# Kernel tuning notes

Hardware: AMD Instinct MI355X
Metric: run time of the kernel (lower is better)

## Reference

```python
import jax, jax.numpy as jnp
import numpy as np

C = 768
H = 12
HD = C // H  # 64


def setup_inputs() -> dict:
    key = jax.random.key(0)
    k1, k2, k3, k4, k5, k6 = jax.random.split(key, 6)
    B, T = 8, 1024
    x = jax.random.normal(k1, (B, T, C), dtype=jnp.float32)
    mask = jax.random.randint(k2, (B, T), 0, 2, dtype=jnp.int32)
    # Linear params stored so that y = x @ W + b (W is [in, out])
    W_attn = jax.random.normal(k3, (C, 3 * C), dtype=jnp.float32) * 0.02
    b_attn = jax.random.normal(k4, (3 * C,), dtype=jnp.float32) * 0.02
    W_proj = jax.random.normal(k5, (C, C), dtype=jnp.float32) * 0.02
    b_proj = jax.random.normal(k6, (C,), dtype=jnp.float32) * 0.02
    return {"x": x, "mask": mask, "W_attn": W_attn, "b_attn": b_attn,
            "W_proj": W_proj, "b_proj": b_proj}


def reference(x, mask, W_attn, b_attn, W_proj, b_proj):
    B, T, _ = x.shape
    qkv = x @ W_attn + b_attn                      # [B, T, 3C]
    q, k, v = jnp.split(qkv, 3, axis=2)            # each [B, T, C]
    # [B, T, C] -> [B, H, T, HD]
    q = q.reshape(B, T, H, HD).transpose(0, 2, 1, 3)
    k = k.reshape(B, T, H, HD).transpose(0, 2, 1, 3)
    v = v.reshape(B, T, H, HD).transpose(0, 2, 1, 3)

    scale = 1.0 / np.sqrt(HD).astype(np.float32)
    att = jnp.einsum('bhqd,bhkd->bhqk', q, k) * scale  # [B, H, T, T]

    causal = jnp.tril(jnp.ones((T, T), dtype=bool))    # [T, T]
    att = jnp.where(causal[None, None], att, -jnp.inf)

    # custom mask: per-(batch, query-row) flag; where mask==0 the whole row
    # of scores is overwritten with 0.0001 (AFTER causal fill, as in torch)
    row_masked = (mask == 0)[:, None, :, None]         # [B, 1, T, 1]
    att = jnp.where(row_masked, jnp.float32(1e-4), att)

    att = jax.nn.softmax(att, axis=-1)
    # dropout layers are identity in eval mode
    y = jnp.einsum('bhqk,bhkd->bhqd', att, v)          # [B, H, T, HD]
    y = y.transpose(0, 2, 1, 3).reshape(B, T, C)
    y = y @ W_proj + b_proj
    return y
```

## Files before the change

kernel.cpp:

```cpp
#include <hip/hip_runtime.h>

#define BQ 8
#define TT 1024
#define CC 768
#define NH 12
#define HD 64
#define BH (BQ*NH)
#define MROWS (BQ*TT)
#define NQKV (3*CC)
#define KD CC

typedef unsigned short u16;
typedef __attribute__((ext_vector_type(4))) short short4v;
typedef __attribute__((ext_vector_type(8))) short short8v;
typedef __attribute__((ext_vector_type(4))) float floatx4;
typedef __attribute__((address_space(1))) const unsigned int gu32;
typedef __attribute__((address_space(3))) unsigned int lu32;

__device__ __forceinline__ float bf2f(u16 u) {
  union { unsigned int i; float f; } c; c.i = ((unsigned int)u) << 16; return c.f;
}
__device__ __forceinline__ u16 f2bf(float f) {
  union { float f; unsigned int i; } c; c.f = f;
  unsigned int i = c.i;
  return (u16)((i + 0x7FFFu + ((i >> 16) & 1u)) >> 16);
}
__device__ __forceinline__ float fast_exp2(float x) {
  return __builtin_amdgcn_exp2f(x);
}
__device__ __forceinline__ void async_ld16(const u16* g, u16* l) {
  __builtin_amdgcn_global_load_lds((gu32*)g, (lu32*)l, 16, 0, 0);
}

#define PREP_CONV 6144
#define PREP_WA   1728

__global__ __launch_bounds__(256) void prep_kernel(
    const float* __restrict__ x, u16* __restrict__ xb,
    const float* __restrict__ Wattn, u16* __restrict__ WtA,
    const float* __restrict__ Wproj, u16* __restrict__ WtP)
{
  __shared__ float tile[32][33];
  int bid = blockIdx.x;
  int tid = threadIdx.x;
  if (bid < PREP_CONV) {
    int i = (bid * 256 + tid) * 4;
    floatx4 v = *(const floatx4*)(x + i);
    short4v o;
    o[0] = (short)f2bf(v[0]); o[1] = (short)f2bf(v[1]);
    o[2] = (short)f2bf(v[2]); o[3] = (short)f2bf(v[3]);
    *(short4v*)(xb + i) = o;
    return;
  }
  const float* in; u16* out; int R, Cc, b2;
  if (bid < PREP_CONV + PREP_WA) { in = Wattn; out = WtA; R = KD; Cc = NQKV; b2 = bid - PREP_CONV; }
  else                           { in = Wproj; out = WtP; R = CC; Cc = CC;   b2 = bid - PREP_CONV - PREP_WA; }
  int ct = Cc >> 5;
  int bx = b2 % ct;
  int by = b2 / ct;
  int tx = tid & 31;
  int ty = tid >> 5;
  int c0 = bx << 5, r0 = by << 5;
#pragma unroll
  for (int s = 0; s < 4; ++s)
    tile[ty + s*8][tx] = in[(size_t)(r0 + ty + s*8) * Cc + c0 + tx];
  __syncthreads();
#pragma unroll
  for (int s = 0; s < 4; ++s)
    out[(size_t)(c0 + ty + s*8) * R + r0 + tx] = f2bf(tile[tx][ty + s*8]);
}

__global__ __launch_bounds__(256) void gemm_bt(
    const u16* __restrict__ A, const u16* __restrict__ Bt,
    const float* __restrict__ bias,
    float* __restrict__ out,
    u16* __restrict__ qo, u16* __restrict__ ko, u16* __restrict__ vo,
    int M, int N, int mode)
{
  __shared__ u16 As[64 * 64];
  __shared__ u16 Bs[128 * 64];

  int tid = threadIdx.x;
  int lane = tid & 63;
  int w = tid >> 6;
  int c = lane & 15;
  int q4 = lane >> 4;

  int mtiles = M >> 6;
  int mt = blockIdx.x % mtiles;
  int nt = blockIdx.x / mtiles;
  int m0 = mt << 6, n0 = nt << 7;

  int wr = (w >> 1) << 5;
  int wc = (w & 1) << 6;

  int srow8 = lane >> 3;
  int ug = ((lane & 7) ^ srow8) << 3;
  const u16* ag = A  + (size_t)(m0 + w * 16 + srow8) * KD + ug;
  const u16* bg = Bt + (size_t)(n0 + w * 32 + srow8) * KD + ug;
  u16* asl = &As[(w * 16) * 64];
  u16* bsl = &Bs[(w * 32) * 64];

  floatx4 acc[2][4];
#pragma unroll
  for (int mi = 0; mi < 2; ++mi)
#pragma unroll
    for (int ni = 0; ni < 4; ++ni) acc[mi][ni] = (floatx4){0.f, 0.f, 0.f, 0.f};

  int c7 = c & 7;

#pragma unroll 1
  for (int kt = 0; kt < KD; kt += 64) {
    async_ld16(ag + kt,              asl);
    async_ld16(ag + kt + 8 * KD,     asl + 8 * 64);
    async_ld16(bg + kt,              bsl);
    async_ld16(bg + kt + 8 * KD,     bsl + 8 * 64);
    async_ld16(bg + kt + 16 * KD,    bsl + 16 * 64);
    async_ld16(bg + kt + 24 * KD,    bsl + 24 * 64);
    __syncthreads();

    short8v af[2][2], bf[4][2];
#pragma unroll
    for (int kc = 0; kc < 2; ++kc) {
      int uoff = ((kc * 4 + q4) ^ c7) << 3;
#pragma unroll
      for (int mi = 0; mi < 2; ++mi)
        af[mi][kc] = *(const short8v*)&As[(wr + mi * 16 + c) * 64 + uoff];
#pragma unroll
      for (int ni = 0; ni < 4; ++ni)
        bf[ni][kc] = *(const short8v*)&Bs[(wc + ni * 16 + c) * 64 + uoff];
    }
#pragma unroll
    for (int kc = 0; kc < 2; ++kc)
#pragma unroll
      for (int mi = 0; mi < 2; ++mi)
#pragma unroll
        for (int ni = 0; ni < 4; ++ni)
          acc[mi][ni] = __builtin_amdgcn_mfma_f32_16x16x32_bf16(af[mi][kc], bf[ni][kc], acc[mi][ni], 0, 0, 0);
    __syncthreads();
  }

  if (mode == 0) {
    int which = (n0 + wc) / CC;
    int nbase = (n0 + wc) - which * CC;
    u16* dst0 = (which == 0) ? qo : ((which == 1) ? ko : vo);
#pragma unroll
    for (int ni = 0; ni < 4; ++ni) {
      int nn = nbase + ni * 16 + c;
      int hh = nn >> 6, dd = nn & 63;
      float bv = bias[which * CC + nn];
#pragma unroll
      for (int mi = 0; mi < 2; ++mi) {
#pragma unroll
        for (int r = 0; r < 4; ++r) {
          int mm = m0 + wr + mi * 16 + q4 * 4 + r;
          int bb = mm >> 10, tt = mm & 1023;
          size_t idx = (((size_t)(bb * NH + hh)) * TT + tt) * HD + dd;
          dst0[idx] = f2bf(acc[mi][ni][r] + bv);
        }
      }
    }
  } else {
#pragma unroll
    for (int ni = 0; ni < 4; ++ni) {
      int nn = n0 + wc + ni * 16 + c;
      float bv = bias[nn];
#pragma unroll
      for (int mi = 0; mi < 2; ++mi) {
#pragma unroll
        for (int r = 0; r < 4; ++r) {
          int mm = m0 + wr + mi * 16 + q4 * 4 + r;
          out[(size_t)mm * N + nn] = acc[mi][ni][r] + bv;
        }
      }
    }
  }
}

__global__ __launch_bounds__(256) void transpose_v(
    const u16* __restrict__ vb, u16* __restrict__ vt)
{
  __shared__ u16 tile[64][72];
  int tid = threadIdx.x;
  int tt0 = (blockIdx.x & 15) << 6;
  int bh = blockIdx.x >> 4;
  {
    int trow = tid >> 2;
    int dchunk = (tid & 3) << 4;
    const u16* src = vb + (((size_t)bh * TT + tt0 + trow) * HD) + dchunk;
    *(short8v*)&tile[trow][dchunk]     = *(const short8v*)src;
    *(short8v*)&tile[trow][dchunk + 8] = *(const short8v*)(src + 8);
  }
  __syncthreads();
  {
    int drow = tid >> 2;
    int tchunk = (tid & 3) << 4;
    short8v a, bv;
#pragma unroll
    for (int j = 0; j < 8; ++j) {
      a[j]  = (short)tile[tchunk + j][drow];
      bv[j] = (short)tile[tchunk + 8 + j][drow];
    }
    u16* dst = vt + ((size_t)bh * HD + drow) * TT + tt0 + tchunk;
    *(short8v*)dst       = a;
    *(short8v*)(dst + 8) = bv;
  }
}

__global__ __launch_bounds__(256) void vk_stats(
    const u16* __restrict__ vtb, const u16* __restrict__ kb,
    float* __restrict__ mv, float* __restrict__ kmaxn)
{
  __shared__ float red[256];
  int bh = blockIdx.x;
  int tid = threadIdx.x;
  int d = tid & 63;
  int g4 = tid >> 6;

  {
    const u16* vp = vtb + ((size_t)bh * HD + d) * TT + g4 * 256;
    float s = 0.f;
#pragma unroll 4
    for (int j = 0; j < 256; j += 8) {
      short8v v = *(const short8v*)(vp + j);
#pragma unroll
      for (int i = 0; i < 8; ++i) s += bf2f((u16)v[i]);
    }
    red[tid] = s;
  }
  __syncthreads();
  if (g4 == 0) mv[bh * HD + d] = (red[d] + red[d + 64] + red[d + 128] + red[d + 192]) * (1.0f / 1024.0f);
  __syncthreads();

  float mx = 0.f;
#pragma unroll 1
  for (int t = tid; t < TT; t += 256) {
    const u16* p = kb + ((size_t)bh * TT + t) * HD;
    float ss = 0.f;
#pragma unroll
    for (int j = 0; j < 64; j += 8) {
      short8v v = *(const short8v*)(p + j);
#pragma unroll
      for (int i = 0; i < 8; ++i) {
        float f = bf2f((u16)v[i]);
        ss = fmaf(f, f, ss);
      }
    }
    mx = fmaxf(mx, ss);
  }
  red[tid] = mx;
  __syncthreads();
  for (int s2 = 128; s2 > 0; s2 >>= 1) {
    if (tid < s2) red[tid] = fmaxf(red[tid], red[tid + s2]);
    __syncthreads();
  }
  if (tid == 0) kmaxn[bh] = sqrtf(red[0]);
}

#define LDW 72
#define SCL 0.18033688f

__global__ __launch_bounds__(256) void attn_kernel(
    const u16* __restrict__ qb, const u16* __restrict__ kb,
    const u16* __restrict__ vtb, const int* __restrict__ mask,
    const float* __restrict__ meanv, const float* __restrict__ kmaxn,
    u16* __restrict__ outb)
{
  __shared__ u16 Ks[64 * LDW];
  __shared__ u16 Vs[64 * LDW];
  __shared__ u16 Ps[4][16 * LDW];

  int tid = threadIdx.x;
  int lane = tid & 63;
  int w = tid >> 6;
  int c = lane & 15;
  int q4 = lane >> 4;

  int pair = blockIdx.x & 7;
  int bh = blockIdx.x >> 3;
  int b = bh / NH;
  int h = bh - b * NH;
  float kmax = kmaxn[bh];

  int srow = tid >> 2;
  int schunk = (tid & 3) << 4;
  const u16* kgp = kb + ((size_t)bh * TT + srow) * HD + schunk;
  const u16* vgp = vtb + ((size_t)bh * HD + srow) * TT + schunk;
  u16* ksw = &Ks[srow * LDW + schunk];
  u16* vsw = &Vs[srow * LDW + schunk];
  u16* pw = &Ps[w][0];

  short8v onesv;
#pragma unroll
  for (int j = 0; j < 8; ++j) onesv[j] = (short)0x3F80;

#pragma unroll 1
  for (int phase = 0; phase < 2; ++phase) {
    int qt = phase ? (15 - pair) : pair;
    int rowbase = (qt << 6) + (w << 4);

    short8v qfrag[2];
    {
      const u16* qp = qb + ((size_t)bh * TT + rowbase + c) * HD + q4 * 8;
      qfrag[0] = *(const short8v*)qp;
      qfrag[1] = *(const short8v*)(qp + 32);
    }

    float q2 = 0.f;
#pragma unroll
    for (int kc = 0; kc < 2; ++kc)
#pragma unroll
      for (int j = 0; j < 8; ++j) {
        float qv = bf2f((u16)qfrag[kc][j]);
        q2 = fmaf(qv, qv, q2);
      }
    q2 += __shfl_xor(q2, 16);
    q2 += __shfl_xor(q2, 32);
    float Mc = sqrtf(q2) * kmax * SCL;

    floatx4 o[4];
#pragma unroll
    for (int i = 0; i < 4; ++i) o[i] = (floatx4){0.f, 0.f, 0.f, 0.f};
    floatx4 o5 = (floatx4){0.f, 0.f, 0.f, 0.f};

    short8v kr0, kr1, vr0, vr1;
    kr0 = *(const short8v*)kgp;
    kr1 = *(const short8v*)(kgp + 8);
    vr0 = *(const short8v*)vgp;
    vr1 = *(const short8v*)(vgp + 8);

#pragma unroll 1
    for (int kt = 0; kt <= qt; ++kt) {
      __syncthreads();
      *(short8v*)ksw = kr0; *(short8v*)(ksw + 8) = kr1;
      *(short8v*)vsw = vr0; *(short8v*)(vsw + 8) = vr1;
      __syncthreads();

      if (kt < qt) {
        const u16* kp = kgp + ((size_t)(kt + 1) << 6) * HD;
        const u16* vp = vgp + ((kt + 1) << 6);
        kr0 = *(const short8v*)kp;
        kr1 = *(const short8v*)(kp + 8);
        vr0 = *(const short8v*)vp;
        vr1 = *(const short8v*)(vp + 8);
      }

      floatx4 s[4];
#pragma unroll
      for (int nt = 0; nt < 4; ++nt) s[nt] = (floatx4){0.f, 0.f, 0.f, 0.f};
#pragma unroll
      for (int kc = 0; kc < 2; ++kc) {
#pragma unroll
        for (int nt = 0; nt < 4; ++nt) {
          short8v kf = *(const short8v*)&Ks[(nt * 16 + c) * LDW + kc * 32 + q4 * 8];
          s[nt] = __builtin_amdgcn_mfma_f32_16x16x32_bf16(kf, qfrag[kc], s[nt], 0, 0, 0);
        }
      }

      int qrl = (w << 4) + c;
#pragma unroll
      for (int nt = 0; nt < 4; ++nt) {
        short4v pk;
#pragma unroll
        for (int r = 0; r < 4; ++r) {
          float sv = s[nt][r];
          if (kt == qt && (nt * 16 + (q4 << 2) + r > qrl)) sv = -INFINITY;
          pk[r] = (short)f2bf(fast_exp2(fmaf(sv, SCL, -Mc)));
        }
        *(short4v*)&pw[c * LDW + nt * 16 + (q4 << 2)] = pk;
      }

#pragma unroll
      for (int kc = 0; kc < 2; ++kc) {
        short8v pf = *(const short8v*)&pw[c * LDW + kc * 32 + q4 * 8];
#pragma unroll
        for (int nt = 0; nt < 4; ++nt) {
          short8v vf = *(const short8v*)&Vs[(nt * 16 + c) * LDW + kc * 32 + q4 * 8];
          o[nt] = __builtin_amdgcn_mfma_f32_16x16x32_bf16(pf, vf, o[nt], 0, 0, 0);
        }
        o5 = __builtin_amdgcn_mfma_f32_16x16x32_bf16(pf, onesv, o5, 0, 0, 0);
      }
    }

    int qrow[4]; bool msk[4]; float inv[4];
#pragma unroll
    for (int r = 0; r < 4; ++r) {
      qrow[r] = rowbase + q4 * 4 + r;
      msk[r] = (mask[b * TT + qrow[r]] == 0);
      inv[r] = 1.f / o5[r];
    }
#pragma unroll
    for (int nt = 0; nt < 4; ++nt) {
      int d = nt * 16 + c;
      float mv = meanv[bh * HD + d];
#pragma unroll
      for (int r = 0; r < 4; ++r) {
        float val = msk[r] ? mv : o[nt][r] * inv[r];
        outb[((size_t)(b * TT + qrow[r])) * CC + h * HD + d] = f2bf(val);
      }
    }
  }
}

extern "C" void kernel_launch(void* const* d_in, const int* in_sizes, int n_in,
                              void* d_out, int out_size, void* d_ws, size_t ws_size,
                              hipStream_t stream)
{
  (void)in_sizes; (void)n_in; (void)out_size; (void)ws_size;
  const float* x     = (const float*)d_in[0];
  const int*   mask  = (const int*)d_in[1];
  const float* Wattn = (const float*)d_in[2];
  const float* battn = (const float*)d_in[3];
  const float* Wproj = (const float*)d_in[4];
  const float* bproj = (const float*)d_in[5];
  float* out = (float*)d_out;

  char* ws = (char*)d_ws;
  size_t off = 0;
  auto alloc = [&](size_t bytes) -> void* {
    void* p = ws + off;
    off += (bytes + 255) & ~(size_t)255;
    return p;
  };
  u16* WtA  = (u16*)alloc((size_t)NQKV * KD * 2);
  u16* WtP  = (u16*)alloc((size_t)CC * CC * 2);
  u16* xb   = (u16*)alloc((size_t)MROWS * CC * 2);
  u16* qbuf = (u16*)alloc((size_t)MROWS * CC * 2);
  u16* kbuf = (u16*)alloc((size_t)MROWS * CC * 2);
  u16* vbuf = (u16*)alloc((size_t)MROWS * CC * 2);
  u16* vtb  = (u16*)alloc((size_t)MROWS * CC * 2);
  u16* abuf = (u16*)alloc((size_t)MROWS * CC * 2);
  float* mv = (float*)alloc((size_t)BH * HD * 4);
  float* kmx = (float*)alloc((size_t)BH * 4);

  prep_kernel<<<8448, 256, 0, stream>>>(x, xb, Wattn, WtA, Wproj, WtP);

  gemm_bt<<<(MROWS/64)*(NQKV/128), 256, 0, stream>>>(
      xb, WtA, battn, nullptr, qbuf, kbuf, vbuf, MROWS, NQKV, 0);

  transpose_v<<<BH * (TT/64), 256, 0, stream>>>(vbuf, vtb);
  vk_stats<<<BH, 256, 0, stream>>>(vtb, kbuf, mv, kmx);

  attn_kernel<<<BH * 8, 256, 0, stream>>>(qbuf, kbuf, vtb, mask, mv, kmx, abuf);

  gemm_bt<<<(MROWS/64)*(CC/128), 256, 0, stream>>>(
      abuf, WtP, bproj, out, nullptr, nullptr, nullptr, MROWS, CC, 1);
}
```

Measured before the change: 200.9 us.

## Fuse V transpose with stats, double-buffer attention K/V, add specialized proj GEMM

```diff
diff --git a/kernel.cpp b/kernel.cpp
--- a/kernel.cpp
+++ b/kernel.cpp
@@ -34,15 +34,23 @@
 
 #define PREP_CONV 6144
 #define PREP_WA   1728
+#define PREP_WP   576
+#define PREP_TOTAL (PREP_CONV + PREP_WA + PREP_WP)
 
 __global__ __launch_bounds__(256) void prep_kernel(
     const float* __restrict__ x, u16* __restrict__ xb,
     const float* __restrict__ Wattn, u16* __restrict__ WtA,
-    const float* __restrict__ Wproj, u16* __restrict__ WtP)
+    const float* __restrict__ Wproj, u16* __restrict__ WtP,
+    float* __restrict__ mvz, unsigned int* __restrict__ kmxz)
 {
   __shared__ float tile[32][33];
   int bid = blockIdx.x;
   int tid = threadIdx.x;
+  if (bid == PREP_TOTAL) {
+    for (int i = tid; i < BH * HD; i += 256) mvz[i] = 0.f;
+    if (tid < BH) kmxz[tid] = 0u;
+    return;
+  }
   if (bid < PREP_CONV) {
     int i = (bid * 256 + tid) * 4;
     floatx4 v = *(const floatx4*)(x + i);
@@ -177,13 +185,101 @@
   }
 }
 
-__global__ __launch_bounds__(256) void transpose_v(
-    const u16* __restrict__ vb, u16* __restrict__ vt)
+__global__ __launch_bounds__(256) void gemm_proj(
+    const u16* __restrict__ A, const u16* __restrict__ Bt,
+    const float* __restrict__ bias, float* __restrict__ out)
+{
+  __shared__ u16 As[64 * 128];
+  __shared__ u16 Bs[128 * 128];
+
+  int tid = threadIdx.x;
+  int lane = tid & 63;
+  int w = tid >> 6;
+  int c = lane & 15;
+  int q4 = lane >> 4;
+
+  int mt = blockIdx.x & 127;
+  int nt = blockIdx.x >> 7;
+  int m0 = mt << 6, n0 = nt << 7;
+
+  int wr = (w >> 1) << 5;
+  int wc = (w & 1) << 6;
+
+  int srow4 = lane >> 4;
+  int u16i = lane & 15;
+
+  floatx4 acc[2][4];
+#pragma unroll
+  for (int mi = 0; mi < 2; ++mi)
+#pragma unroll
+    for (int ni = 0; ni < 4; ++ni) acc[mi][ni] = (floatx4){0.f, 0.f, 0.f, 0.f};
+
+#pragma unroll 1
+  for (int kt = 0; kt < KD; kt += 128) {
+#pragma unroll
+    for (int i = 0; i < 4; ++i) {
+      int row = w * 16 + i * 4 + srow4;
+      async_ld16(A + (size_t)(m0 + row) * KD + kt + ((u16i ^ (row & 15)) << 3),
+                 &As[(w * 16 + i * 4) * 128]);
+    }
+#pragma unroll
+    for (int i = 0; i < 8; ++i) {
+      int row = w * 32 + i * 4 + srow4;
+      async_ld16(Bt + (size_t)(n0 + row) * KD + kt + ((u16i ^ (row & 15)) << 3),
+                 &Bs[(w * 32 + i * 4) * 128]);
+    }
+    __syncthreads();
+
+#pragma unroll
+    for (int kc = 0; kc < 4; ++kc) {
+      int uoff = (((kc << 2) + q4) ^ c) << 3;
+      short8v af0 = *(const short8v*)&As[(wr + c) * 128 + uoff];
+      short8v af1 = *(const short8v*)&As[(wr + 16 + c) * 128 + uoff];
+      short8v bf0 = *(const short8v*)&Bs[(wc + c) * 128 + uoff];
+      short8v bf1 = *(const short8v*)&Bs[(wc + 16 + c) * 128 + uoff];
+      short8v bf2 = *(const short8v*)&Bs[(wc + 32 + c) * 128 + uoff];
+      short8v bf3 = *(const short8v*)&Bs[(wc + 48 + c) * 128 + uoff];
+      acc[0][0] = __builtin_amdgcn_mfma_f32_16x16x32_bf16(af0, bf0, acc[0][0], 0, 0, 0);
+      acc[0][1] = __builtin_amdgcn_mfma_f32_16x16x32_bf16(af0, bf1, acc[0][1], 0, 0, 0);
+      acc[0][2] = __builtin_amdgcn_mfma_f32_16x16x32_bf16(af0, bf2, acc[0][2], 0, 0, 0);
+      acc[0][3] = __builtin_amdgcn_mfma_f32_16x16x32_bf16(af0, bf3, acc[0][3], 0, 0, 0);
+      acc[1][0] = __builtin_amdgcn_mfma_f32_16x16x32_bf16(af1, bf0, acc[1][0], 0, 0, 0);
+      acc[1][1] = __builtin_amdgcn_mfma_f32_16x16x32_bf16(af1, bf1, acc[1][1], 0, 0, 0);
+      acc[1][2] = __builtin_amdgcn_mfma_f32_16x16x32_bf16(af1, bf2, acc[1][2], 0, 0, 0);
+      acc[1][3] = __builtin_amdgcn_mfma_f32_16x16x32_bf16(af1, bf3, acc[1][3], 0, 0, 0);
+    }
+    __syncthreads();
+  }
+
+#pragma unroll
+  for (int ni = 0; ni < 4; ++ni) {
+    int nn = n0 + wc + ni * 16 + c;
+    float bv = bias[nn];
+#pragma unroll
+    for (int mi = 0; mi < 2; ++mi) {
+#pragma unroll
+      for (int r = 0; r < 4; ++r) {
+        int mm = m0 + wr + mi * 16 + q4 * 4 + r;
+        out[(size_t)mm * CC + nn] = acc[mi][ni][r] + bv;
+      }
+    }
+  }
+}
+
+__global__ __launch_bounds__(256) void tvstats(
+    const u16* __restrict__ vb, u16* __restrict__ vt,
+    const u16* __restrict__ kb,
+    float* __restrict__ mvp, unsigned int* __restrict__ kmxp)
 {
   __shared__ u16 tile[64][72];
+  __shared__ float red[256];
+  __shared__ float rmax4[4];
   int tid = threadIdx.x;
+  int lane = tid & 63;
+  int w = tid >> 6;
   int tt0 = (blockIdx.x & 15) << 6;
   int bh = blockIdx.x >> 4;
+
   {
     int trow = tid >> 2;
     int dchunk = (tid & 3) << 4;
@@ -191,7 +287,31 @@
     *(short8v*)&tile[trow][dchunk]     = *(const short8v*)src;
     *(short8v*)&tile[trow][dchunk + 8] = *(const short8v*)(src + 8);
   }
+  {
+    int tr = tid >> 2;
+    int dq = (tid & 3) << 4;
+    const u16* kp = kb + ((size_t)bh * TT + tt0 + tr) * HD + dq;
+    short8v a = *(const short8v*)kp;
+    short8v b2 = *(const short8v*)(kp + 8);
+    float ss = 0.f;
+#pragma unroll
+    for (int i = 0; i < 8; ++i) {
+      float f0 = bf2f((u16)a[i]), f1 = bf2f((u16)b2[i]);
+      ss = fmaf(f0, f0, ss); ss = fmaf(f1, f1, ss);
+    }
+    ss += __shfl_xor(ss, 1);
+    ss += __shfl_xor(ss, 2);
+    float rm = ss;
+    rm = fmaxf(rm, __shfl_xor(rm, 4));
+    rm = fmaxf(rm, __shfl_xor(rm, 8));
+    rm = fmaxf(rm, __shfl_xor(rm, 16));
+    rm = fmaxf(rm, __shfl_xor(rm, 32));
+    if (lane == 0) rmax4[w] = rm;
+  }
   __syncthreads();
+  if (tid == 0)
+    atomicMax(&kmxp[bh], __float_as_uint(fmaxf(fmaxf(rmax4[0], rmax4[1]),
+                                               fmaxf(rmax4[2], rmax4[3]))));
   {
     int drow = tid >> 2;
     int tchunk = (tid & 3) << 4;
@@ -205,56 +325,17 @@
     *(short8v*)dst       = a;
     *(short8v*)(dst + 8) = bv;
   }
-}
-
-__global__ __launch_bounds__(256) void vk_stats(
-    const u16* __restrict__ vtb, const u16* __restrict__ kb,
-    float* __restrict__ mv, float* __restrict__ kmaxn)
-{
-  __shared__ float red[256];
-  int bh = blockIdx.x;
-  int tid = threadIdx.x;
-  int d = tid & 63;
-  int g4 = tid >> 6;
-
   {
-    const u16* vp = vtb + ((size_t)bh * HD + d) * TT + g4 * 256;
+    int d = tid & 63;
+    int g = tid >> 6;
     float s = 0.f;
-#pragma unroll 4
-    for (int j = 0; j < 256; j += 8) {
-      short8v v = *(const short8v*)(vp + j);
-#pragma unroll
-      for (int i = 0; i < 8; ++i) s += bf2f((u16)v[i]);
-    }
+#pragma unroll
+    for (int j = 0; j < 16; ++j) s += bf2f(tile[g * 16 + j][d]);
     red[tid] = s;
   }
   __syncthreads();
-  if (g4 == 0) mv[bh * HD + d] = (red[d] + red[d + 64] + red[d + 128] + red[d + 192]) * (1.0f / 1024.0f);
-  __syncthreads();
-
-  float mx = 0.f;
-#pragma unroll 1
-  for (int t = tid; t < TT; t += 256) {
-    const u16* p = kb + ((size_t)bh * TT + t) * HD;
-    float ss = 0.f;
-#pragma unroll
-    for (int j = 0; j < 64; j += 8) {
-      short8v v = *(const short8v*)(p + j);
-#pragma unroll
-      for (int i = 0; i < 8; ++i) {
-        float f = bf2f((u16)v[i]);
-        ss = fmaf(f, f, ss);
-      }
-    }
-    mx = fmaxf(mx, ss);
-  }
-  red[tid] = mx;
-  __syncthreads();
-  for (int s2 = 128; s2 > 0; s2 >>= 1) {
-    if (tid < s2) red[tid] = fmaxf(red[tid], red[tid + s2]);
-    __syncthreads();
-  }
-  if (tid == 0) kmaxn[bh] = sqrtf(red[0]);
+  if (tid < 64)
+    atomicAdd(&mvp[bh * HD + tid], red[tid] + red[tid + 64] + red[tid + 128] + red[tid + 192]);
 }
 
 #define LDW 72
@@ -263,11 +344,11 @@
 __global__ __launch_bounds__(256) void attn_kernel(
     const u16* __restrict__ qb, const u16* __restrict__ kb,
     const u16* __restrict__ vtb, const int* __restrict__ mask,
-    const float* __restrict__ meanv, const float* __restrict__ kmaxn,
+    const float* __restrict__ meanv, const unsigned int* __restrict__ kmaxn,
     u16* __restrict__ outb)
 {
-  __shared__ u16 Ks[64 * LDW];
-  __shared__ u16 Vs[64 * LDW];
+  __shared__ u16 Ks[2][64 * LDW];
+  __shared__ u16 Vs[2][64 * LDW];
   __shared__ u16 Ps[4][16 * LDW];
 
   int tid = threadIdx.x;
@@ -280,14 +361,12 @@
   int bh = blockIdx.x >> 3;
   int b = bh / NH;
   int h = bh - b * NH;
-  float kmax = kmaxn[bh];
+  float kmax = sqrtf(__uint_as_float(kmaxn[bh]));
 
   int srow = tid >> 2;
   int schunk = (tid & 3) << 4;
   const u16* kgp = kb + ((size_t)bh * TT + srow) * HD + schunk;
   const u16* vgp = vtb + ((size_t)bh * HD + srow) * TT + schunk;
-  u16* ksw = &Ks[srow * LDW + schunk];
-  u16* vsw = &Vs[srow * LDW + schunk];
   u16* pw = &Ps[w][0];
 
   short8v onesv;
@@ -323,17 +402,21 @@
     for (int i = 0; i < 4; ++i) o[i] = (floatx4){0.f, 0.f, 0.f, 0.f};
     floatx4 o5 = (floatx4){0.f, 0.f, 0.f, 0.f};
 
-    short8v kr0, kr1, vr0, vr1;
-    kr0 = *(const short8v*)kgp;
-    kr1 = *(const short8v*)(kgp + 8);
-    vr0 = *(const short8v*)vgp;
-    vr1 = *(const short8v*)(vgp + 8);
+    short8v kr0 = *(const short8v*)kgp;
+    short8v kr1 = *(const short8v*)(kgp + 8);
+    short8v vr0 = *(const short8v*)vgp;
+    short8v vr1 = *(const short8v*)(vgp + 8);
+    __syncthreads();
+    {
+      u16* kd = &Ks[0][srow * LDW + schunk];
+      u16* vd = &Vs[0][srow * LDW + schunk];
+      *(short8v*)kd = kr0; *(short8v*)(kd + 8) = kr1;
+      *(short8v*)vd = vr0; *(short8v*)(vd + 8) = vr1;
+    }
 
 #pragma unroll 1
     for (int kt = 0; kt <= qt; ++kt) {
-      __syncthreads();
-      *(short8v*)ksw = kr0; *(short8v*)(ksw + 8) = kr1;
-      *(short8v*)vsw = vr0; *(short8v*)(vsw + 8) = vr1;
+      int cur = kt & 1;
       __syncthreads();
 
       if (kt < qt) {
@@ -348,14 +431,16 @@
       floatx4 s[4];
 #pragma unroll
       for (int nt = 0; nt < 4; ++nt) s[nt] = (floatx4){0.f, 0.f, 0.f, 0.f};
+      __builtin_amdgcn_s_setprio(1);
 #pragma unroll
       for (int kc = 0; kc < 2; ++kc) {
 #pragma unroll
         for (int nt = 0; nt < 4; ++nt) {
-          short8v kf = *(const short8v*)&Ks[(nt * 16 + c) * LDW + kc * 32 + q4 * 8];
+          short8v kf = *(const short8v*)&Ks[cur][(nt * 16 + c) * LDW + kc * 32 + q4 * 8];
           s[nt] = __builtin_amdgcn_mfma_f32_16x16x32_bf16(kf, qfrag[kc], s[nt], 0, 0, 0);
         }
       }
+      __builtin_amdgcn_s_setprio(0);
 
       int qrl = (w << 4) + c;
 #pragma unroll
@@ -370,16 +455,25 @@
         *(short4v*)&pw[c * LDW + nt * 16 + (q4 << 2)] = pk;
       }
 
+      if (kt < qt) {
+        u16* kd = &Ks[cur ^ 1][srow * LDW + schunk];
+        u16* vd = &Vs[cur ^ 1][srow * LDW + schunk];
+        *(short8v*)kd = kr0; *(short8v*)(kd + 8) = kr1;
+        *(short8v*)vd = vr0; *(short8v*)(vd + 8) = vr1;
+      }
+
+      __builtin_amdgcn_s_setprio(1);
 #pragma unroll
       for (int kc = 0; kc < 2; ++kc) {
         short8v pf = *(const short8v*)&pw[c * LDW + kc * 32 + q4 * 8];
 #pragma unroll
         for (int nt = 0; nt < 4; ++nt) {
-          short8v vf = *(const short8v*)&Vs[(nt * 16 + c) * LDW + kc * 32 + q4 * 8];
+          short8v vf = *(const short8v*)&Vs[cur][(nt * 16 + c) * LDW + kc * 32 + q4 * 8];
           o[nt] = __builtin_amdgcn_mfma_f32_16x16x32_bf16(pf, vf, o[nt], 0, 0, 0);
         }
         o5 = __builtin_amdgcn_mfma_f32_16x16x32_bf16(pf, onesv, o5, 0, 0, 0);
       }
+      __builtin_amdgcn_s_setprio(0);
     }
 
     int qrow[4]; bool msk[4]; float inv[4];
@@ -392,7 +486,7 @@
 #pragma unroll
     for (int nt = 0; nt < 4; ++nt) {
       int d = nt * 16 + c;
-      float mv = meanv[bh * HD + d];
+      float mv = meanv[bh * HD + d] * 0.0009765625f;
 #pragma unroll
       for (int r = 0; r < 4; ++r) {
         float val = msk[r] ? mv : o[nt][r] * inv[r];
@@ -431,18 +525,16 @@
   u16* vtb  = (u16*)alloc((size_t)MROWS * CC * 2);
   u16* abuf = (u16*)alloc((size_t)MROWS * CC * 2);
   float* mv = (float*)alloc((size_t)BH * HD * 4);
-  float* kmx = (float*)alloc((size_t)BH * 4);
-
-  prep_kernel<<<8448, 256, 0, stream>>>(x, xb, Wattn, WtA, Wproj, WtP);
+  unsigned int* kmx = (unsigned int*)alloc((size_t)BH * 4);
+
+  prep_kernel<<<PREP_TOTAL + 1, 256, 0, stream>>>(x, xb, Wattn, WtA, Wproj, WtP, mv, kmx);
 
   gemm_bt<<<(MROWS/64)*(NQKV/128), 256, 0, stream>>>(
       xb, WtA, battn, nullptr, qbuf, kbuf, vbuf, MROWS, NQKV, 0);
 
-  transpose_v<<<BH * (TT/64), 256, 0, stream>>>(vbuf, vtb);
-  vk_stats<<<BH, 256, 0, stream>>>(vtb, kbuf, mv, kmx);
+  tvstats<<<BH * 16, 256, 0, stream>>>(vbuf, vtb, kbuf, mv, kmx);
 
   attn_kernel<<<BH * 8, 256, 0, stream>>>(qbuf, kbuf, vtb, mask, mv, kmx, abuf);
 
-  gemm_bt<<<(MROWS/64)*(CC/128), 256, 0, stream>>>(
-      abuf, WtP, bproj, out, nullptr, nullptr, nullptr, MROWS, CC, 1);
-}
+  gemm_proj<<<(MROWS/64)*(CC/128), 256, 0, stream>>>(abuf, WtP, bproj, out);
+}
```

New measurement: 196.9 us. 1.02x faster.
